# Optimization experiments

Measured on AMD Instinct MI355X. Metric: run time of the kernel, lower is better.

## Reference

```python
import jax, jax.numpy as jnp
import numpy as np

N = 100000
IN_C = 128
OUT_C = 128
HEADS = 4
C = OUT_C // HEADS  # per-head channels = 32
E = 1600000
EPS_BN = 1e-5
NEG_SLOPE = 0.2


def setup_inputs() -> dict:
    key = jax.random.key(0)
    ks = jax.random.split(key, 16)
    x = jax.random.normal(ks[0], (N, IN_C), dtype=jnp.float32)
    edge_index = jax.random.randint(ks[1], (2, E), 0, N, dtype=jnp.int64)
    s = 0.05
    params = {
        'W1': jax.random.normal(ks[2], (IN_C, HEADS * C), jnp.float32) * s,
        'a_src1': jax.random.normal(ks[3], (HEADS, C), jnp.float32) * s,
        'a_dst1': jax.random.normal(ks[4], (HEADS, C), jnp.float32) * s,
        'b1': jax.random.normal(ks[5], (HEADS * C,), jnp.float32) * s,
        'gamma1': jnp.ones((OUT_C,), jnp.float32),
        'beta1': jnp.zeros((OUT_C,), jnp.float32),
        'W2': jax.random.normal(ks[6], (OUT_C, HEADS * C), jnp.float32) * s,
        'a_src2': jax.random.normal(ks[7], (HEADS, C), jnp.float32) * s,
        'a_dst2': jax.random.normal(ks[8], (HEADS, C), jnp.float32) * s,
        'b2': jax.random.normal(ks[9], (HEADS * C,), jnp.float32) * s,
        'gamma2': jnp.ones((OUT_C,), jnp.float32),
        'beta2': jnp.zeros((OUT_C,), jnp.float32),
    }
    return {'x': x, 'edge_index': edge_index, **params}


def _gat_conv(x, src, dst, W, a_src, a_dst, b):
    # x: [N, F_in]; src/dst: [E'] (self-loops already appended)
    n = x.shape[0]
    h = (x @ W).reshape(n, HEADS, C)                      # [N, H, C]
    alpha_s = jnp.sum(h * a_src, axis=-1)                 # [N, H]
    alpha_d = jnp.sum(h * a_dst, axis=-1)                 # [N, H]
    logits = alpha_s[src] + alpha_d[dst]                  # [E', H]
    logits = jnp.where(logits >= 0, logits, NEG_SLOPE * logits)
    # segment softmax over incoming edges of each destination node
    m = jax.ops.segment_max(logits, dst, num_segments=n)  # [N, H]
    e = jnp.exp(logits - m[dst])
    denom = jax.ops.segment_sum(e, dst, num_segments=n)   # [N, H]
    alpha = e / (denom[dst] + 1e-16)                      # [E', H]
    msg = alpha[:, :, None] * h[src]                      # [E', H, C]
    out = jax.ops.segment_sum(msg, dst, num_segments=n)   # [N, H, C]
    return out.reshape(n, HEADS * C) + b


def _batch_norm(h, gamma, beta):
    mean = jnp.mean(h, axis=0)
    var = jnp.var(h, axis=0)
    return (h - mean) * jax.lax.rsqrt(var + EPS_BN) * gamma + beta


def reference(x, edge_index, W1, a_src1, a_dst1, b1, gamma1, beta1,
              W2, a_src2, a_dst2, b2, gamma2, beta2):
    # PyG GATConv default: add self-loops
    loops = jnp.arange(N, dtype=edge_index.dtype)
    src = jnp.concatenate([edge_index[0], loops])
    dst = jnp.concatenate([edge_index[1], loops])

    out = _gat_conv(x, src, dst, W1, a_src1, a_dst1, b1)
    out = jax.nn.relu(_batch_norm(out, gamma1, beta1))
    out = _gat_conv(out, src, dst, W2, a_src2, a_dst2, b2)
    out = _batch_norm(out, gamma2, beta2)
    return jax.nn.relu(out + x)  # skip is Identity since in_channels == out_channels
```

## Files before the change

### kernel.cpp

```cpp
#include <hip/hip_runtime.h>

#define MAXNB 1024
#define NSLOT 8

typedef __attribute__((ext_vector_type(8))) short bf8;
typedef __attribute__((ext_vector_type(4))) float f32x4;

__device__ __forceinline__ unsigned pack_bf16x2(float a, float b) {
  unsigned ua = __float_as_uint(a);
  ua = (ua + 0x7fffu + ((ua >> 16) & 1u)) >> 16;
  unsigned ub = __float_as_uint(b);
  ub = (ub + 0x7fffu + ((ub >> 16) & 1u)) >> 16;
  return ua | (ub << 16);
}

__global__ __launch_bounds__(256) void k_wprep(const float* __restrict__ W1,
                                               uint4* __restrict__ Wf1,
                                               const float* __restrict__ W2,
                                               uint4* __restrict__ Wf2) {
  const int half = blockIdx.x >> 3;
  const float* W = half ? W2 : W1;
  uint4* Wf = half ? Wf2 : Wf1;
  const int t = (blockIdx.x & 7) * 256 + threadIdx.x;
  const int frag = t >> 6, lane = t & 63;
  const int ct = frag >> 2, kc = frag & 3;
  const int col = ct * 16 + (lane & 15);
  const int k0 = kc * 32 + (lane >> 4) * 8;
  unsigned p[4];
#pragma unroll
  for (int j = 0; j < 4; ++j)
    p[j] = pack_bf16x2(W[(k0 + 2 * j) * 128 + col],
                       W[(k0 + 2 * j + 1) * 128 + col]);
  Wf[t] = make_uint4(p[0], p[1], p[2], p[3]);
}

__global__ __launch_bounds__(256) void k_gemm(
    const float* __restrict__ X, const uint4* __restrict__ Wf,
    unsigned* __restrict__ Hb, int n, const float* __restrict__ stats,
    const float* __restrict__ gamma, const float* __restrict__ beta,
    float invN, const float* __restrict__ a_src,
    const float* __restrict__ a_dst, float* __restrict__ as_,
    float* __restrict__ ad_) {
  __shared__ float stag[64 * 132];
  __shared__ float ssl[256];
  const int tid = threadIdx.x;
  if (stats && tid < 128) {
    float s = 0.f, s2 = 0.f;
#pragma unroll
    for (int k = 0; k < NSLOT; ++k) {
      s += stats[k * 256 + tid];
      s2 += stats[k * 256 + 128 + tid];
    }
    float mean = s * invN;
    float var = s2 * invN - mean * mean;
    float sc = gamma[tid] * rsqrtf(var + 1e-5f);
    ssl[tid] = sc;
    ssl[128 + tid] = beta[tid] - mean * sc;
  }
  __syncthreads();

  const int w = tid >> 6, lane = tid & 63;
  const int q = lane >> 4, nl = lane & 15;
  const long row0 = (long)blockIdx.x * 64;
  long rowA = row0 + w * 16 + nl;
  if (rowA >= n) rowA = n - 1;

  bf8 a[4];
#pragma unroll
  for (int kc = 0; kc < 4; ++kc) {
    const float* p = X + rowA * 128 + kc * 32 + q * 8;
    float4 v0 = *(const float4*)p;
    float4 v1 = *(const float4*)(p + 4);
    if (stats) {
      const int kb = kc * 32 + q * 8;
      float4 s0 = *(const float4*)&ssl[kb];
      float4 s1 = *(const float4*)&ssl[kb + 4];
      float4 h0 = *(const float4*)&ssl[128 + kb];
      float4 h1 = *(const float4*)&ssl[128 + kb + 4];
      v0.x = fmaxf(fmaf(v0.x, s0.x, h0.x), 0.f);
      v0.y = fmaxf(fmaf(v0.y, s0.y, h0.y), 0.f);
      v0.z = fmaxf(fmaf(v0.z, s0.z, h0.z), 0.f);
      v0.w = fmaxf(fmaf(v0.w, s0.w, h0.w), 0.f);
      v1.x = fmaxf(fmaf(v1.x, s1.x, h1.x), 0.f);
      v1.y = fmaxf(fmaf(v1.y, s1.y, h1.y), 0.f);
      v1.z = fmaxf(fmaf(v1.z, s1.z, h1.z), 0.f);
      v1.w = fmaxf(fmaf(v1.w, s1.w, h1.w), 0.f);
    }
    union { uint4 u; bf8 v; } cv;
    cv.u = make_uint4(pack_bf16x2(v0.x, v0.y), pack_bf16x2(v0.z, v0.w),
                      pack_bf16x2(v1.x, v1.y), pack_bf16x2(v1.z, v1.w));
    a[kc] = cv.v;
  }

  f32x4 acc[8];
#pragma unroll
  for (int ct = 0; ct < 8; ++ct) {
    f32x4 c = {0.f, 0.f, 0.f, 0.f};
#pragma unroll
    for (int kc = 0; kc < 4; ++kc) {
      union { uint4 u; bf8 v; } b;
      b.u = Wf[(ct * 4 + kc) * 64 + lane];
      c = __builtin_amdgcn_mfma_f32_16x16x32_bf16(a[kc], b.v, c, 0, 0, 0);
    }
    acc[ct] = c;
  }

  const int lr = w * 16 + q * 4;
#pragma unroll
  for (int ct = 0; ct < 8; ++ct)
#pragma unroll
    for (int r = 0; r < 4; ++r)
      stag[(lr + r) * 132 + ct * 16 + nl] = acc[ct][r];
  __syncthreads();

  {
    const int row = tid >> 2, seg = tid & 3;
    const long grow = row0 + row;
    if (grow < n) {
      float sp = 0.f, dp = 0.f;
      const float* p = &stag[row * 132 + seg * 32];
#pragma unroll
      for (int i = 0; i < 8; ++i) {
        float4 h4 = *(const float4*)(p + i * 4);
        float4 s4 = ((const float4*)a_src)[seg * 8 + i];
        float4 d4 = ((const float4*)a_dst)[seg * 8 + i];
        sp += h4.x * s4.x + h4.y * s4.y + h4.z * s4.z + h4.w * s4.w;
        dp += h4.x * d4.x + h4.y * d4.y + h4.z * d4.z + h4.w * d4.w;
        uint2 o;
        o.x = pack_bf16x2(h4.x, h4.y);
        o.y = pack_bf16x2(h4.z, h4.w);
        ((uint2*)Hb)[grow * 32 + seg * 8 + i] = o;
      }
      as_[grow * 4 + seg] = sp;
      ad_[grow * 4 + seg] = dp;
    }
  }
}

__global__ __launch_bounds__(256) void k_hist(const int* __restrict__ ei,
                                              int E, int NB,
                                              int* __restrict__ bcnt) {
  __shared__ int hist[MAXNB];
  for (int i = threadIdx.x; i < NB; i += 256) hist[i] = 0;
  __syncthreads();
  const int e0 = blockIdx.x * 4096;
#pragma unroll
  for (int k = 0; k < 16; ++k) {
    int e = e0 + k * 256 + threadIdx.x;
    if (e < E) atomicAdd(&hist[ei[E + e] >> 7], 1);
  }
  __syncthreads();
  for (int i = threadIdx.x; i < NB; i += 256) {
    int c = hist[i];
    if (c) atomicAdd(&bcnt[i], c);
  }
}

__global__ __launch_bounds__(1024) void k_bprefix(const int* __restrict__ bcnt,
                                                  int NB,
                                                  int* __restrict__ bstart,
                                                  int* __restrict__ bcur) {
  __shared__ int sh[1024];
  const int t = threadIdx.x;
  int v = (t < NB) ? bcnt[t] : 0;
  sh[t] = v;
  __syncthreads();
  for (int off = 1; off < 1024; off <<= 1) {
    int u = (t >= off) ? sh[t - off] : 0;
    __syncthreads();
    sh[t] += u;
    __syncthreads();
  }
  if (t < NB) {
    int ex = sh[t] - v;
    bstart[t] = ex;
    bcur[t] = ex;
    if (t == NB - 1) bstart[NB] = sh[t];
  }
}

__global__ __launch_bounds__(256) void k_scatter(const int* __restrict__ ei,
                                                 int E, int NB,
                                                 int* __restrict__ bcur,
                                                 int* __restrict__ packed) {
  __shared__ int hist[MAXNB];
  __shared__ int hbase[MAXNB];
  for (int i = threadIdx.x; i < NB; i += 256) hist[i] = 0;
  __syncthreads();
  const int e0 = blockIdx.x * 4096;
  int myb[16], myv[16];
#pragma unroll
  for (int k = 0; k < 16; ++k) {
    int e = e0 + k * 256 + threadIdx.x;
    myb[k] = -1;
    myv[k] = 0;
    if (e < E) {
      int s = ei[e], d = ei[E + e];
      myb[k] = d >> 7;
      myv[k] = (s << 7) | (d & 127);
      atomicAdd(&hist[myb[k]], 1);
    }
  }
  __syncthreads();
  for (int i = threadIdx.x; i < NB; i += 256) {
    int c = hist[i];
    hbase[i] = c ? atomicAdd(&bcur[i], c) : 0;
    hist[i] = 0;
  }
  __syncthreads();
#pragma unroll
  for (int k = 0; k < 16; ++k) {
    if (myb[k] >= 0) {
      int p = hbase[myb[k]] + atomicAdd(&hist[myb[k]], 1);
      packed[p] = myv[k];
    }
  }
}

__global__ __launch_bounds__(256) void k_local(const int* __restrict__ packed,
                                               const int* __restrict__ bstart,
                                               int n, int* __restrict__ srcs,
                                               int* __restrict__ offs,
                                               int* __restrict__ deg) {
  const int b = blockIdx.x;
  const int node0 = b << 7;
  const int nn = min(128, n - node0);
  const int e0 = bstart[b], e1 = bstart[b + 1];
  __shared__ int dcnt[128], cur[128], scan[128];
  const int tid = threadIdx.x;
  if (tid < 128) dcnt[tid] = 0;
  __syncthreads();
  for (int i = e0 + tid; i < e1; i += 256)
    atomicAdd(&dcnt[packed[i] & 127], 1);
  __syncthreads();
  int v = 0;
  if (tid < 128) {
    v = (tid < nn) ? dcnt[tid] + 1 : 0;
    scan[tid] = v;
  }
  __syncthreads();
  for (int off = 1; off < 128; off <<= 1) {
    int u = 0;
    if (tid < 128 && tid >= off) u = scan[tid - off];
    __syncthreads();
    if (tid < 128) scan[tid] += u;
    __syncthreads();
  }
  if (tid < nn) {
    const int o = e0 + node0 + (scan[tid] - v);
    offs[node0 + tid] = o;
    deg[node0 + tid] = dcnt[tid];
    srcs[o] = node0 + tid;
    cur[tid] = o + 1;
  }
  __syncthreads();
  for (int i = e0 + tid; i < e1; i += 256) {
    const int pv = packed[i];
    const int p = atomicAdd(&cur[pv & 127], 1);
    srcs[p] = pv >> 7;
  }
}

__global__ __launch_bounds__(256) void k_agg(
    const int* __restrict__ offs, const int* __restrict__ deg,
    const int* __restrict__ srcs, const uint4* __restrict__ Hb,
    const float* __restrict__ as_, const float* __restrict__ ad_,
    float* __restrict__ out, float* __restrict__ stats, int n) {
  __shared__ float sblk[4][2][128];
  const int tid = threadIdx.x;
  const int node = blockIdx.x * 16 + (tid >> 4);
  const bool active = node < n;
  const int w = tid >> 6, lane = tid & 63;
  const int t = lane & 15;
  const int th = t >> 2;
  const int j4 = lane & 3;
  const int o0 = active ? offs[node] : 0;
  const int dg = active ? deg[node] + 1 : 1;
  const float adv = active ? ad_[node * 4 + th] : 0.f;

  float den = 0.f;
  float acc[8];
#pragma unroll
  for (int i = 0; i < 8; ++i) acc[i] = 0.f;

#define LOADSE(J, S, EV)                               \
  {                                                    \
    const int j_ = (J);                                \
    S = srcs[o0 + (j_ < dg ? j_ : 0)];                 \
    float l_ = as_[S * 4 + th] + adv;                  \
    l_ = l_ >= 0.f ? l_ : 0.2f * l_;                   \
    EV = (j_ < dg) ? __expf(fminf(l_, 80.f)) : 0.f;    \
  }

#define GATHER(DST, SREG, JJ)                                            \
  {                                                                      \
    int ss_ = __builtin_amdgcn_ds_swizzle((SREG), ((JJ) << 5) | 0x10);   \
    DST = Hb[(long)ss_ * 16 + t];                                        \
  }

#define FMA8(HV, JJ, EREG)                                                 \
  {                                                                        \
    float wv_ = __uint_as_float(__builtin_amdgcn_ds_swizzle(               \
        __float_as_int(EREG), ((JJ) << 5) | 0x1C));                        \
    acc[0] = fmaf(wv_, __uint_as_float(HV.x << 16), acc[0]);               \
    acc[1] = fmaf(wv_, __uint_as_float(HV.x & 0xffff0000u), acc[1]);       \
    acc[2] = fmaf(wv_, __uint_as_float(HV.y << 16), acc[2]);               \
    acc[3] = fmaf(wv_, __uint_as_float(HV.y & 0xffff0000u), acc[3]);       \
    acc[4] = fmaf(wv_, __uint_as_float(HV.z << 16), acc[4]);               \
    acc[5] = fmaf(wv_, __uint_as_float(HV.z & 0xffff0000u), acc[5]);       \
    acc[6] = fmaf(wv_, __uint_as_float(HV.w << 16), acc[6]);               \
    acc[7] = fmaf(wv_, __uint_as_float(HV.w & 0xffff0000u), acc[7]);       \
  }

  int s_c, s_n, s_f;
  float e_c, e_n, e_f;
  LOADSE(j4, s_c, e_c);
  LOADSE(4 + j4, s_n, e_n);
  uint4 h0, h1, h2, h3;
  GATHER(h0, s_c, 0);
  GATHER(h1, s_c, 1);
  GATHER(h2, s_c, 2);
  GATHER(h3, s_c, 3);

  for (int base = 0; base < dg; base += 4) {
    LOADSE(base + 8 + j4, s_f, e_f);
    uint4 g0, g1, g2, g3;
    GATHER(g0, s_n, 0);
    GATHER(g1, s_n, 1);
    GATHER(g2, s_n, 2);
    GATHER(g3, s_n, 3);
    den += e_c;
    FMA8(h0, 0, e_c);
    FMA8(h1, 1, e_c);
    FMA8(h2, 2, e_c);
    FMA8(h3, 3, e_c);
    s_c = s_n; e_c = e_n;
    s_n = s_f; e_n = e_f;
    h0 = g0; h1 = g1; h2 = g2; h3 = g3;
  }
#undef LOADSE
#undef GATHER
#undef FMA8

  den += __shfl_xor(den, 1, 64);
  den += __shfl_xor(den, 2, 64);
  const float invden = 1.f / (den + 1e-16f);
  float sums[8], sqs[8];
#pragma unroll
  for (int i = 0; i < 8; ++i) {
    float v = acc[i] * invden;
    acc[i] = v;
    sums[i] = v;
    sqs[i] = v * v;
  }
  if (active) {
    float4 o0v = make_float4(acc[0], acc[1], acc[2], acc[3]);
    float4 o1v = make_float4(acc[4], acc[5], acc[6], acc[7]);
    ((float4*)out)[(long)node * 32 + t * 2] = o0v;
    ((float4*)out)[(long)node * 32 + t * 2 + 1] = o1v;
  }
#pragma unroll
  for (int off = 16; off <= 32; off <<= 1) {
#pragma unroll
    for (int i = 0; i < 8; ++i) {
      sums[i] += __shfl_xor(sums[i], off, 64);
      sqs[i] += __shfl_xor(sqs[i], off, 64);
    }
  }
  if (lane < 16) {
#pragma unroll
    for (int i = 0; i < 8; ++i) {
      sblk[w][0][lane * 8 + i] = sums[i];
      sblk[w][1][lane * 8 + i] = sqs[i];
    }
  }
  __syncthreads();
  {
    const int c = tid & 127, sidx = tid >> 7;
    float v = sblk[0][sidx][c] + sblk[1][sidx][c] + sblk[2][sidx][c] +
              sblk[3][sidx][c];
    atomicAdd(&stats[(blockIdx.x & (NSLOT - 1)) * 256 + sidx * 128 + c], v);
  }
}

__global__ __launch_bounds__(256) void k_bn_apply(
    const float* __restrict__ V, const float* __restrict__ stats,
    const float* __restrict__ gamma, const float* __restrict__ beta,
    float invN, const float* __restrict__ skip, float* __restrict__ Y,
    int total4) {
  __shared__ float ssl[256];
  const int tid = threadIdx.x;
  if (tid < 128) {
    float s = 0.f, s2 = 0.f;
#pragma unroll
    for (int k = 0; k < NSLOT; ++k) {
      s += stats[k * 256 + tid];
      s2 += stats[k * 256 + 128 + tid];
    }
    float mean = s * invN;
    float var = s2 * invN - mean * mean;
    float sc = gamma[tid] * rsqrtf(var + 1e-5f);
    ssl[tid] = sc;
    ssl[128 + tid] = beta[tid] - mean * sc;
  }
  __syncthreads();
  for (int i = blockIdx.x * 256 + tid; i < total4; i += gridDim.x * 256) {
    const int c4 = i & 31;
    float4 v = ((const float4*)V)[i];
    float4 sc = *(const float4*)&ssl[c4 * 4];
    float4 sh = *(const float4*)&ssl[128 + c4 * 4];
    float4 s = ((const float4*)skip)[i];
    float4 y;
    y.x = fmaxf(fmaf(v.x, sc.x, sh.x) + s.x, 0.f);
    y.y = fmaxf(fmaf(v.y, sc.y, sh.y) + s.y, 0.f);
    y.z = fmaxf(fmaf(v.z, sc.z, sh.z) + s.z, 0.f);
    y.w = fmaxf(fmaf(v.w, sc.w, sh.w) + s.w, 0.f);
    ((float4*)Y)[i] = y;
  }
}

extern "C" void kernel_launch(void* const* d_in, const int* in_sizes, int n_in,
                              void* d_out, int out_size, void* d_ws,
                              size_t ws_size, hipStream_t stream) {
  const float* x = (const float*)d_in[0];
  const int* ei = (const int*)d_in[1];
  const float* W1 = (const float*)d_in[2];
  const float* a_src1 = (const float*)d_in[3];
  const float* a_dst1 = (const float*)d_in[4];
  const float* gamma1 = (const float*)d_in[6];
  const float* beta1 = (const float*)d_in[7];
  const float* W2 = (const float*)d_in[8];
  const float* a_src2 = (const float*)d_in[9];
  const float* a_dst2 = (const float*)d_in[10];
  const float* gamma2 = (const float*)d_in[12];
  const float* beta2 = (const float*)d_in[13];

  const int n = in_sizes[0] / 128;
  const int E = in_sizes[1] / 2;
  const int EP = E + n;
  const int NB = (n + 127) >> 7;
  const int EB = (E + 4095) / 4096;
  const float invN = 1.0f / (float)n;

  char* w = (char*)d_ws;
  const size_t szNC = (size_t)n * 128 * sizeof(float);
  unsigned* Hb = (unsigned*)w;  w += (size_t)n * 64 * sizeof(unsigned);
  float* Bagg = (float*)w;      w += szNC;
  float* as_ = (float*)w;       w += (size_t)n * 4 * sizeof(float);
  float* ad_ = (float*)w;       w += (size_t)n * 4 * sizeof(float);
  int* srcs = (int*)w;          w += (size_t)EP * sizeof(int);
  int* packed = (int*)w;        w += (size_t)E * sizeof(int);
  int* deg = (int*)w;           w += (size_t)n * sizeof(int);
  int* offs = (int*)w;          w += (size_t)n * sizeof(int);
  int* bstart = (int*)w;        w += (size_t)(NB + 1) * sizeof(int);
  int* bcur = (int*)w;          w += (size_t)NB * sizeof(int);
  uint4* Wf1 = (uint4*)w;       w += 2048 * sizeof(uint4);
  uint4* Wf2 = (uint4*)w;       w += 2048 * sizeof(uint4);
  char* zreg = w;
  int* bcnt = (int*)w;          w += (size_t)NB * sizeof(int);
  float* stats1 = (float*)w;    w += NSLOT * 256 * sizeof(float);
  float* stats2 = (float*)w;    w += NSLOT * 256 * sizeof(float);
  const size_t zbytes = (size_t)(w - zreg);

  hipMemsetAsync(zreg, 0, zbytes, stream);

  k_wprep<<<16, 256, 0, stream>>>(W1, Wf1, W2, Wf2);

  k_hist<<<EB, 256, 0, stream>>>(ei, E, NB, bcnt);
  k_bprefix<<<1, 1024, 0, stream>>>(bcnt, NB, bstart, bcur);
  k_scatter<<<EB, 256, 0, stream>>>(ei, E, NB, bcur, packed);
  k_local<<<NB, 256, 0, stream>>>(packed, bstart, n, srcs, offs, deg);

  k_gemm<<<(n + 63) / 64, 256, 0, stream>>>(x, Wf1, Hb, n, nullptr, nullptr,
                                            nullptr, invN, a_src1, a_dst1,
                                            as_, ad_);
  k_agg<<<(n + 15) / 16, 256, 0, stream>>>(offs, deg, srcs, (const uint4*)Hb,
                                           as_, ad_, Bagg, stats1, n);

  k_gemm<<<(n + 63) / 64, 256, 0, stream>>>(Bagg, Wf2, Hb, n, stats1, gamma1,
                                            beta1, invN, a_src2, a_dst2, as_,
                                            ad_);
  k_agg<<<(n + 15) / 16, 256, 0, stream>>>(offs, deg, srcs, (const uint4*)Hb,
                                           as_, ad_, Bagg, stats2, n);
  k_bn_apply<<<2048, 256, 0, stream>>>(Bagg, stats2, gamma2, beta2, invN, x,
                                       (float*)d_out, n * 32);
}
```

Measured before the change: 440.3 us.

## Split aggregation work per head with 4-lane node groups and interleaved block mapping

The aggregation kernel now assigns each block one head for a 64-node tile, with 4 lanes per node-head instead of 16 lanes per node across all heads. Blocks are ordered so that the four heads of neighbouring tiles run close together, which should help L2 reuse of the source indices. The software-pipelined prefetch of gathered features is dropped in favour of a simpler one-stage loop. The aim is less divergence waste on variable degree and better per-head locality, but it risks more edge-list and logit reloads (4x) and more gather latency exposure.

```diff
diff --git a/kernel.cpp b/kernel.cpp
--- a/kernel.cpp
+++ b/kernel.cpp
@@ -265,18 +265,24 @@
     const int* __restrict__ offs, const int* __restrict__ deg,
     const int* __restrict__ srcs, const uint4* __restrict__ Hb,
     const float* __restrict__ as_, const float* __restrict__ ad_,
-    float* __restrict__ out, float* __restrict__ stats, int n) {
-  __shared__ float sblk[4][2][128];
+    float* __restrict__ out, float* __restrict__ stats, int n, int ntiles) {
+  __shared__ float sblk[4][2][32];
   const int tid = threadIdx.x;
-  const int node = blockIdx.x * 16 + (tid >> 4);
+  const int bid = blockIdx.x;
+  const int head = (bid & 7) >> 1;
+  const int tile = ((bid >> 3) << 1) | (bid & 1);
+  if (tile >= ntiles) return;
+  const int w = tid >> 6, lane = tid & 63;
+  const int unit = tid >> 2;
+  const int node = tile * 64 + unit;
   const bool active = node < n;
-  const int w = tid >> 6, lane = tid & 63;
-  const int t = lane & 15;
-  const int th = t >> 2;
-  const int j4 = lane & 3;
+  const int t4 = lane & 3;
   const int o0 = active ? offs[node] : 0;
-  const int dg = active ? deg[node] + 1 : 1;
-  const float adv = active ? ad_[node * 4 + th] : 0.f;
+  const int dg = active ? deg[node] + 1 : 0;
+  const float adv = active ? ad_[node * 4 + head] : 0.f;
+  const int* sp = srcs + o0;
+  const uint4* Hp = Hb + head * 4 + t4;
+  const float* asH = as_ + head;
 
   float den = 0.f;
   float acc[8];
@@ -286,16 +292,16 @@
 #define LOADSE(J, S, EV)                               \
   {                                                    \
     const int j_ = (J);                                \
-    S = srcs[o0 + (j_ < dg ? j_ : 0)];                 \
-    float l_ = as_[S * 4 + th] + adv;                  \
+    S = sp[j_ < dg ? j_ : 0];                          \
+    float l_ = asH[S * 4] + adv;                       \
     l_ = l_ >= 0.f ? l_ : 0.2f * l_;                   \
     EV = (j_ < dg) ? __expf(fminf(l_, 80.f)) : 0.f;    \
   }
 
 #define GATHER(DST, SREG, JJ)                                            \
   {                                                                      \
-    int ss_ = __builtin_amdgcn_ds_swizzle((SREG), ((JJ) << 5) | 0x10);   \
-    DST = Hb[(long)ss_ * 16 + t];                                        \
+    int ss_ = __builtin_amdgcn_ds_swizzle((SREG), ((JJ) << 5) | 0x1C);   \
+    DST = Hp[(long)ss_ * 16];                                            \
   }
 
 #define FMA8(HV, JJ, EREG)                                                 \
@@ -312,31 +318,24 @@
     acc[7] = fmaf(wv_, __uint_as_float(HV.w & 0xffff0000u), acc[7]);       \
   }
 
-  int s_c, s_n, s_f;
-  float e_c, e_n, e_f;
-  LOADSE(j4, s_c, e_c);
-  LOADSE(4 + j4, s_n, e_n);
-  uint4 h0, h1, h2, h3;
-  GATHER(h0, s_c, 0);
-  GATHER(h1, s_c, 1);
-  GATHER(h2, s_c, 2);
-  GATHER(h3, s_c, 3);
+  int s_c, s_n;
+  float e_c, e_n;
+  LOADSE(t4, s_c, e_c);
 
   for (int base = 0; base < dg; base += 4) {
-    LOADSE(base + 8 + j4, s_f, e_f);
-    uint4 g0, g1, g2, g3;
-    GATHER(g0, s_n, 0);
-    GATHER(g1, s_n, 1);
-    GATHER(g2, s_n, 2);
-    GATHER(g3, s_n, 3);
+    LOADSE(base + 4 + t4, s_n, e_n);
     den += e_c;
+    uint4 h0, h1, h2, h3;
+    GATHER(h0, s_c, 0);
+    GATHER(h1, s_c, 1);
+    GATHER(h2, s_c, 2);
+    GATHER(h3, s_c, 3);
     FMA8(h0, 0, e_c);
     FMA8(h1, 1, e_c);
     FMA8(h2, 2, e_c);
     FMA8(h3, 3, e_c);
-    s_c = s_n; e_c = e_n;
-    s_n = s_f; e_n = e_f;
-    h0 = g0; h1 = g1; h2 = g2; h3 = g3;
+    s_c = s_n;
+    e_c = e_n;
   }
 #undef LOADSE
 #undef GATHER
@@ -356,18 +355,18 @@
   if (active) {
     float4 o0v = make_float4(acc[0], acc[1], acc[2], acc[3]);
     float4 o1v = make_float4(acc[4], acc[5], acc[6], acc[7]);
-    ((float4*)out)[(long)node * 32 + t * 2] = o0v;
-    ((float4*)out)[(long)node * 32 + t * 2 + 1] = o1v;
-  }
-#pragma unroll
-  for (int off = 16; off <= 32; off <<= 1) {
+    ((float4*)out)[(long)node * 32 + head * 8 + t4 * 2] = o0v;
+    ((float4*)out)[(long)node * 32 + head * 8 + t4 * 2 + 1] = o1v;
+  }
+#pragma unroll
+  for (int off = 4; off <= 32; off <<= 1) {
 #pragma unroll
     for (int i = 0; i < 8; ++i) {
       sums[i] += __shfl_xor(sums[i], off, 64);
       sqs[i] += __shfl_xor(sqs[i], off, 64);
     }
   }
-  if (lane < 16) {
+  if (lane < 4) {
 #pragma unroll
     for (int i = 0; i < 8; ++i) {
       sblk[w][0][lane * 8 + i] = sums[i];
@@ -375,11 +374,12 @@
     }
   }
   __syncthreads();
-  {
-    const int c = tid & 127, sidx = tid >> 7;
+  if (tid < 64) {
+    const int c = tid & 31, sidx = tid >> 5;
     float v = sblk[0][sidx][c] + sblk[1][sidx][c] + sblk[2][sidx][c] +
               sblk[3][sidx][c];
-    atomicAdd(&stats[(blockIdx.x & (NSLOT - 1)) * 256 + sidx * 128 + c], v);
+    atomicAdd(&stats[(bid & (NSLOT - 1)) * 256 + sidx * 128 + head * 32 + c],
+              v);
   }
 }
 
@@ -471,17 +471,20 @@
   k_scatter<<<EB, 256, 0, stream>>>(ei, E, NB, bcur, packed);
   k_local<<<NB, 256, 0, stream>>>(packed, bstart, n, srcs, offs, deg);
 
+  const int ntiles = (n + 63) >> 6;
+  const int nagg = 8 * ((ntiles + 1) >> 1);
+
   k_gemm<<<(n + 63) / 64, 256, 0, stream>>>(x, Wf1, Hb, n, nullptr, nullptr,
                                             nullptr, invN, a_src1, a_dst1,
                                             as_, ad_);
-  k_agg<<<(n + 15) / 16, 256, 0, stream>>>(offs, deg, srcs, (const uint4*)Hb,
-                                           as_, ad_, Bagg, stats1, n);
+  k_agg<<<nagg, 256, 0, stream>>>(offs, deg, srcs, (const uint4*)Hb, as_, ad_,
+                                  Bagg, stats1, n, ntiles);
 
   k_gemm<<<(n + 63) / 64, 256, 0, stream>>>(Bagg, Wf2, Hb, n, stats1, gamma1,
                                             beta1, invN, a_src2, a_dst2, as_,
                                             ad_);
-  k_agg<<<(n + 15) / 16, 256, 0, stream>>>(offs, deg, srcs, (const uint4*)Hb,
-                                           as_, ad_, Bagg, stats2, n);
+  k_agg<<<nagg, 256, 0, stream>>>(offs, deg, srcs, (const uint4*)Hb, as_, ad_,
+                                  Bagg, stats2, n, ntiles);
   k_bn_apply<<<2048, 256, 0, stream>>>(Bagg, stats2, gamma2, beta2, invN, x,
                                        (float*)d_out, n * 32);
 }
```

Result: slower. 584.5 us (+32.8%).
